# Kernel optimization log

Hardware: AMD Instinct MI355X
Metric: run time of the kernel (lower is better)

## Reference

```python
import jax, jax.numpy as jnp
import numpy as np

TOTAL = 262144
FEAT = 512
NSEG = 1024


def setup_inputs() -> dict:
    key = jax.random.key(0)
    k1, k2 = jax.random.split(key)
    batch = jax.random.normal(k1, (TOTAL, FEAT), dtype=jnp.float32)
    segment_ids = jnp.sort(jax.random.randint(k2, (TOTAL,), 0, NSEG)).astype(jnp.int32)
    return {"batch": batch, "segment_ids": segment_ids, "num_segments": NSEG}


def reference(batch, segment_ids, num_segments):
    # mode='mean', keep_shape=True: per-segment mean, broadcast back to rows.
    seg_sum = jax.ops.segment_sum(batch, segment_ids, num_segments=num_segments)
    counts = jax.ops.segment_sum(
        jnp.ones((batch.shape[0],), dtype=batch.dtype), segment_ids,
        num_segments=num_segments)
    means = seg_sum / jnp.maximum(counts, 1.0)[:, None]  # [NSEG, FEAT]
    out = jnp.take(means, segment_ids, axis=0)           # keep_shape expand
    return out
```

## Files before the change

### kernel.cpp

```cpp
#include <hip/hip_runtime.h>

#define FEAT 512
#define F4 (FEAT / 4)
#define NSEG 1024

__global__ void seg_bounds_kernel(const int* __restrict__ seg,
                                  int* __restrict__ starts, int total) {
    int i = blockIdx.x * blockDim.x + threadIdx.x;
    if (i >= total) return;
    int cur = seg[i];
    int prev = (i == 0) ? -1 : seg[i - 1];
    for (int s = prev + 1; s <= cur; ++s) starts[s] = i;
    if (i == total - 1) {
        for (int s = cur + 1; s <= NSEG; ++s) starts[s] = total;
    }
}

__global__ __launch_bounds__(512) void seg_mean_kernel(const float* __restrict__ batch,
                                                       const int* __restrict__ starts,
                                                       float* __restrict__ out) {
    const int s      = blockIdx.x;
    const int tid    = threadIdx.x;
    const int lane_f = tid & (F4 - 1);
    const int rgrp   = tid >> 7;

    const int start = starts[s];
    const int end   = starts[s + 1];
    const int count = end - start;

    const float4* b4 = (const float4*)batch;
    float4 acc = make_float4(0.f, 0.f, 0.f, 0.f);
    for (int r = start + rgrp; r < end; r += 4) {
        float4 v = b4[(size_t)r * F4 + lane_f];
        acc.x += v.x; acc.y += v.y; acc.z += v.z; acc.w += v.w;
    }

    __shared__ float4 red[4][F4];
    red[rgrp][lane_f] = acc;
    __syncthreads();

    if (rgrp == 0) {
        float4 a = red[0][lane_f];
        float4 b = red[1][lane_f];
        float4 c = red[2][lane_f];
        float4 d = red[3][lane_f];
        const float inv = 1.0f / (float)(count > 0 ? count : 1);
        float4 m;
        m.x = (a.x + b.x + c.x + d.x) * inv;
        m.y = (a.y + b.y + c.y + d.y) * inv;
        m.z = (a.z + b.z + c.z + d.z) * inv;
        m.w = (a.w + b.w + c.w + d.w) * inv;
        red[0][lane_f] = m;
    }
    __syncthreads();

    const float4 mean = red[0][lane_f];
    float4* o4 = (float4*)out;
    for (int r = start + rgrp; r < end; r += 4) {
        o4[(size_t)r * F4 + lane_f] = mean;
    }
}

extern "C" void kernel_launch(void* const* d_in, const int* in_sizes, int n_in,
                              void* d_out, int out_size, void* d_ws, size_t ws_size,
                              hipStream_t stream) {
    const float* batch = (const float*)d_in[0];
    const int*   seg   = (const int*)d_in[1];
    float*       out   = (float*)d_out;
    const int total    = in_sizes[1];

    int* starts = (int*)d_ws;

    seg_bounds_kernel<<<(total + 255) / 256, 256, 0, stream>>>(seg, starts, total);
    seg_mean_kernel<<<NSEG, 512, 0, stream>>>(batch, starts, out);
}
```

Measured before the change: 243.8 us.

## Split segment mean into chunked atomic partial sums and a separate broadcast pass

```diff
diff --git a/kernel.cpp b/kernel.cpp
--- a/kernel.cpp
+++ b/kernel.cpp
@@ -1,8 +1,9 @@
 #include <hip/hip_runtime.h>
 
 #define FEAT 512
-#define F4 (FEAT / 4)
+#define F4   128
 #define NSEG 1024
+#define CHUNK 128
 
 __global__ void seg_bounds_kernel(const int* __restrict__ seg,
                                   int* __restrict__ starts, int total) {
@@ -16,9 +17,70 @@
     }
 }
 
-__global__ __launch_bounds__(512) void seg_mean_kernel(const float* __restrict__ batch,
-                                                       const int* __restrict__ starts,
-                                                       float* __restrict__ out) {
+__global__ void inv_count_kernel(const int* __restrict__ starts,
+                                 float* __restrict__ invcnt) {
+    int s = blockIdx.x * blockDim.x + threadIdx.x;
+    if (s < NSEG) {
+        int c = starts[s + 1] - starts[s];
+        invcnt[s] = 1.0f / (float)(c > 0 ? c : 1);
+    }
+}
+
+__global__ __launch_bounds__(128) void seg_partial_kernel(const float* __restrict__ batch,
+                                                          const int* __restrict__ seg,
+                                                          const int* __restrict__ starts,
+                                                          float* __restrict__ sums,
+                                                          int total) {
+    const int tid = threadIdx.x;
+    const int r0 = blockIdx.x * CHUNK;
+    if (r0 >= total) return;
+    const int r1 = min(r0 + CHUNK, total);
+
+    const float4* b4 = (const float4*)batch;
+    const int s0 = seg[r0];
+    const int s1 = seg[r1 - 1];
+
+    for (int s = s0; s <= s1; ++s) {
+        const int a = max(starts[s], r0);
+        const int b = min(starts[s + 1], r1);
+        if (a >= b) continue;
+        float4 acc = make_float4(0.f, 0.f, 0.f, 0.f);
+        for (int r = a; r < b; ++r) {
+            float4 v = b4[(size_t)r * F4 + tid];
+            acc.x += v.x; acc.y += v.y; acc.z += v.z; acc.w += v.w;
+        }
+        float* dst = sums + (size_t)s * FEAT + tid * 4;
+        atomicAdd(dst + 0, acc.x);
+        atomicAdd(dst + 1, acc.y);
+        atomicAdd(dst + 2, acc.z);
+        atomicAdd(dst + 3, acc.w);
+    }
+}
+
+__global__ __launch_bounds__(256) void broadcast_kernel(const int* __restrict__ seg,
+                                                        const float* __restrict__ sums,
+                                                        const float* __restrict__ invcnt,
+                                                        float* __restrict__ out,
+                                                        int total) {
+    const float4* s4 = (const float4*)sums;
+    float4* o4 = (float4*)out;
+    const size_t nf4 = (size_t)total * F4;
+    const size_t stride = (size_t)gridDim.x * blockDim.x;
+    for (size_t idx = (size_t)blockIdx.x * blockDim.x + threadIdx.x;
+         idx < nf4; idx += stride) {
+        const int row = (int)(idx >> 7);
+        const int col = (int)(idx & 127);
+        const int s   = seg[row];
+        const float ic = invcnt[s];
+        float4 m = s4[(size_t)s * F4 + col];
+        m.x *= ic; m.y *= ic; m.z *= ic; m.w *= ic;
+        o4[idx] = m;
+    }
+}
+
+__global__ __launch_bounds__(512) void seg_mean_fused_kernel(const float* __restrict__ batch,
+                                                             const int* __restrict__ starts,
+                                                             float* __restrict__ out) {
     const int s      = blockIdx.x;
     const int tid    = threadIdx.x;
     const int lane_f = tid & (F4 - 1);
@@ -69,8 +131,26 @@
     float*       out   = (float*)d_out;
     const int total    = in_sizes[1];
 
-    int* starts = (int*)d_ws;
+    const size_t sums_bytes   = (size_t)NSEG * FEAT * sizeof(float);
+    const size_t starts_off   = sums_bytes;
+    const size_t invcnt_off   = sums_bytes + 8192;
+    const size_t need         = invcnt_off + NSEG * sizeof(float);
 
-    seg_bounds_kernel<<<(total + 255) / 256, 256, 0, stream>>>(seg, starts, total);
-    seg_mean_kernel<<<NSEG, 512, 0, stream>>>(batch, starts, out);
+    if (ws_size >= need) {
+        float* sums   = (float*)d_ws;
+        int*   starts = (int*)((char*)d_ws + starts_off);
+        float* invcnt = (float*)((char*)d_ws + invcnt_off);
+
+        hipMemsetAsync(sums, 0, sums_bytes, stream);
+        seg_bounds_kernel<<<(total + 255) / 256, 256, 0, stream>>>(seg, starts, total);
+        inv_count_kernel<<<NSEG / 256, 256, 0, stream>>>(starts, invcnt);
+
+        const int nchunks = (total + CHUNK - 1) / CHUNK;
+        seg_partial_kernel<<<nchunks, 128, 0, stream>>>(batch, seg, starts, sums, total);
+        broadcast_kernel<<<2048, 256, 0, stream>>>(seg, sums, invcnt, out, total);
+    } else {
+        int* starts = (int*)d_ws;
+        seg_bounds_kernel<<<(total + 255) / 256, 256, 0, stream>>>(seg, starts, total);
+        seg_mean_fused_kernel<<<NSEG, 512, 0, stream>>>(batch, starts, out);
+    }
 }
```

Result: slower. 288.1 us (+18.2%).

## Split segment mean into reduce kernel plus grid-wide broadcast kernel

Applied to the files above, without the earlier changes.

```diff
diff --git a/kernel.cpp b/kernel.cpp
--- a/kernel.cpp
+++ b/kernel.cpp
@@ -1,7 +1,7 @@
 #include <hip/hip_runtime.h>
 
 #define FEAT 512
-#define F4 (FEAT / 4)
+#define F4   128
 #define NSEG 1024
 
 __global__ void seg_bounds_kernel(const int* __restrict__ seg,
@@ -18,7 +18,62 @@
 
 __global__ __launch_bounds__(512) void seg_mean_kernel(const float* __restrict__ batch,
                                                        const int* __restrict__ starts,
-                                                       float* __restrict__ out) {
+                                                       float* __restrict__ means) {
+    const int s      = blockIdx.x;
+    const int tid    = threadIdx.x;
+    const int lane_f = tid & (F4 - 1);
+    const int rgrp   = tid >> 7;
+
+    const int start = starts[s];
+    const int end   = starts[s + 1];
+    const int count = end - start;
+
+    const float4* b4 = (const float4*)batch;
+    float4 acc = make_float4(0.f, 0.f, 0.f, 0.f);
+    for (int r = start + rgrp; r < end; r += 4) {
+        float4 v = b4[(size_t)r * F4 + lane_f];
+        acc.x += v.x; acc.y += v.y; acc.z += v.z; acc.w += v.w;
+    }
+
+    __shared__ float4 red[4][F4];
+    red[rgrp][lane_f] = acc;
+    __syncthreads();
+
+    if (rgrp == 0) {
+        float4 a = red[0][lane_f];
+        float4 b = red[1][lane_f];
+        float4 c = red[2][lane_f];
+        float4 d = red[3][lane_f];
+        const float inv = 1.0f / (float)(count > 0 ? count : 1);
+        float4 m;
+        m.x = (a.x + b.x + c.x + d.x) * inv;
+        m.y = (a.y + b.y + c.y + d.y) * inv;
+        m.z = (a.z + b.z + c.z + d.z) * inv;
+        m.w = (a.w + b.w + c.w + d.w) * inv;
+        ((float4*)means)[(size_t)s * F4 + lane_f] = m;
+    }
+}
+
+__global__ __launch_bounds__(256) void broadcast_kernel(const int* __restrict__ seg,
+                                                        const float* __restrict__ means,
+                                                        float* __restrict__ out,
+                                                        int total) {
+    const float4* m4 = (const float4*)means;
+    float4* o4 = (float4*)out;
+    const size_t nf4 = (size_t)total * F4;
+    const size_t stride = (size_t)gridDim.x * blockDim.x;
+    for (size_t idx = (size_t)blockIdx.x * blockDim.x + threadIdx.x;
+         idx < nf4; idx += stride) {
+        const int row = (int)(idx >> 7);
+        const int col = (int)(idx & 127);
+        const int s   = seg[row];
+        o4[idx] = m4[(size_t)s * F4 + col];
+    }
+}
+
+__global__ __launch_bounds__(512) void seg_mean_fused_kernel(const float* __restrict__ batch,
+                                                             const int* __restrict__ starts,
+                                                             float* __restrict__ out) {
     const int s      = blockIdx.x;
     const int tid    = threadIdx.x;
     const int lane_f = tid & (F4 - 1);
@@ -69,8 +124,20 @@
     float*       out   = (float*)d_out;
     const int total    = in_sizes[1];
 
-    int* starts = (int*)d_ws;
+    const size_t means_bytes = (size_t)NSEG * FEAT * sizeof(float);
+    const size_t starts_off  = means_bytes;
+    const size_t need        = starts_off + (NSEG + 1) * sizeof(int);
 
-    seg_bounds_kernel<<<(total + 255) / 256, 256, 0, stream>>>(seg, starts, total);
-    seg_mean_kernel<<<NSEG, 512, 0, stream>>>(batch, starts, out);
+    if (ws_size >= need) {
+        float* means  = (float*)d_ws;
+        int*   starts = (int*)((char*)d_ws + starts_off);
+
+        seg_bounds_kernel<<<(total + 255) / 256, 256, 0, stream>>>(seg, starts, total);
+        seg_mean_kernel<<<NSEG, 512, 0, stream>>>(batch, starts, means);
+        broadcast_kernel<<<2048, 256, 0, stream>>>(seg, means, out, total);
+    } else {
+        int* starts = (int*)d_ws;
+        seg_bounds_kernel<<<(total + 255) / 256, 256, 0, stream>>>(seg, starts, total);
+        seg_mean_fused_kernel<<<NSEG, 512, 0, stream>>>(batch, starts, out);
+    }
 }
```

After: 283.3 us. +16.2%, slower.
